# Kernel optimization log

Measured on AMD Instinct MI355X. Metric: run time of the kernel, lower is better.

Reference implementation:

```python
import jax, jax.numpy as jnp
import numpy as np

WIDTH = 11
SIGMA = 5.0
C1 = 0.01 ** 2
C2 = 0.02 ** 2
B, C, H, W = 16, 3, 512, 512


def _gaussian_kernel(n_channel):
    # Matches torch module: exp(-x^2/(2 sigma^2)) over arange(-width/2, width/2)
    g = np.exp(-1.0 * np.arange(-(WIDTH / 2), WIDTH / 2) ** 2 / (2 * SIGMA ** 2))
    g = np.outer(g, g.reshape(WIDTH, 1))
    g = g / np.sum(g)
    # Original kernel is block-diagonal [C, C, k, k] with w on the diagonal;
    # mathematically identical to a depthwise conv with kernel [C, 1, k, k].
    w = np.zeros((n_channel, 1, WIDTH, WIDTH), dtype=np.float32)
    w[:, 0] = g.astype(np.float32)
    return jnp.asarray(w)


def setup_inputs() -> dict:
    key = jax.random.key(0)
    k1, k2 = jax.random.split(key)
    inp = jax.random.normal(k1, (B, C, H, W), dtype=jnp.float32)
    tgt = jax.random.normal(k2, (B, C, H, W), dtype=jnp.float32)
    return {"input": inp, "target": tgt, "w": _gaussian_kernel(C)}


def reference(input, target, w):
    nb, nc = input.shape[0], input.shape[1]

    def blur(x):  # depthwise VALID conv == original block-diagonal dense conv
        return jax.lax.conv_general_dilated(
            x, w, window_strides=(1, 1), padding='VALID',
            dimension_numbers=('NCHW', 'OIHW', 'NCHW'),
            feature_group_count=nc)

    mux = blur(input)
    muy = blur(target)
    sigmax2 = blur(input * input) - mux * mux
    sigmay2 = blur(target * target) - muy * muy
    sigmaxy = blur(input * target) - mux * muy

    l = (2 * mux * muy + C1) / (mux * mux + muy * muy + C1)
    cs = (2 * sigmaxy + C2) / (sigmax2 + sigmay2 + C2)
    return 1 - jnp.sum(l * cs) / (nb * nc)
```

## Files before the change

kernel.cpp:

```cpp
#include <hip/hip_runtime.h>

typedef __attribute__((ext_vector_type(8))) _Float16 f16x8;
typedef __attribute__((ext_vector_type(4))) float f32x4;
typedef __attribute__((ext_vector_type(4))) _Float16 h4;
typedef __attribute__((ext_vector_type(2))) __fp16 hw2;
typedef __attribute__((ext_vector_type(2))) float v2f;

#define IMG 512
#define OUT_N 502
#define NPLANE 48
#define NBAND 32
#define NBLK (NBAND * NPLANE)
#define VP 520
#define C1c 0.0001f
#define C2c 0.0004f

union H8u { hw2 p[4]; f16x8 v; };
union H4u { hw2 p[2]; h4 v; };

__device__ __forceinline__ float ssim_px(float mx, float my, float P, float M) {
    float A = mx*mx, B = my*my, mxy = mx*my;
    float sumsq = 0.5f*(P+M) - A - B;
    float sxy   = 0.25f*(P-M) - mxy;
    float num = (2.f*mxy + C1c) * (2.f*sxy + C2c);
    float den = (A + B + C1c) * (sumsq + C2c);
    return num * __builtin_amdgcn_rcpf(den);
}

__device__ __forceinline__ float ssim_px2(v2f mx, v2f my, v2f P, v2f M) {
    v2f A = mx*mx, B = my*my, mxy = mx*my;
    v2f sumsq = 0.5f*(P+M) - A - B;
    v2f sxy   = 0.25f*(P-M) - mxy;
    v2f num = (2.f*mxy + C1c) * (2.f*sxy + C2c);
    v2f den = (A + B + C1c) * (sumsq + C2c);
    return num.x * __builtin_amdgcn_rcpf(den.x)
         + num.y * __builtin_amdgcn_rcpf(den.y);
}

__global__ __launch_bounds__(512, 2) void ssim_band(
    const float* __restrict__ in, const float* __restrict__ tgt,
    const float* __restrict__ w, float* __restrict__ partial)
{
    __shared__ __attribute__((aligned(16))) _Float16 vlds[4][16][VP];
    __shared__ float g1s[16];
    __shared__ float red[8];

    const int tid   = threadIdx.x;
    const int lane  = tid & 63;
    const int wv    = tid >> 6;
    const int f     = blockIdx.x;
    const int s     = ((f & 7) * (NBLK / 8)) + (f >> 3);
    const int band  = s & (NBAND - 1);
    const int plane = s >> 5;
    const int r0 = band * 16;
    const bool edge = (r0 + 16 > OUT_N);
    const float* __restrict__ ip = in  + (size_t)plane * (IMG*IMG);
    const float* __restrict__ tp = tgt + (size_t)plane * (IMG*IMG);

    const int fi = lane & 15;
    const int kg = lane >> 4;
    const int kB = kg * 8;

    int idx[8];
    #pragma unroll
    for (int q = 0; q < 8; ++q) {
        const int rr = min(r0 + kB + q, IMG - 1);
        idx[q] = rr * IMG + wv * 64 + fi;
    }

#define VLOAD(T, XS, YS) \
    { _Pragma("unroll") \
      for (int q = 0; q < 8; ++q) { \
          XS[q] = ip[idx[q] + 16*(T)]; \
          YS[q] = tp[idx[q] + 16*(T)]; \
      } }

    float xA[8], yA[8], xB[8], yB[8];
    VLOAD(0, xA, yA)
    VLOAD(1, xB, yB)

    if (tid < 11) {
        float ws_ = 0.f;
        #pragma unroll
        for (int j = 0; j < 11; ++j) ws_ += w[tid*11 + j];
        g1s[tid] = ws_;
    }
    __syncthreads();
    float g[11];
    #pragma unroll
    for (int j = 0; j < 11; ++j)
        g[j] = __int_as_float(__builtin_amdgcn_readfirstlane(__float_as_int(g1s[j])));

    f16x8 band_f;
    #pragma unroll
    for (int q = 0; q < 8; ++q) {
        float wq = 0.f;
        #pragma unroll
        for (int j = 0; j <= 10; ++j)
            wq = (kB + q - fi == j) ? g[j] : wq;
        band_f[q] = (_Float16)wq;
    }

    float acc = 0.f;
    const f32x4 z = {0.f, 0.f, 0.f, 0.f};

#define VSTORE(F, D) \
    { H4u u_; \
      u_.p[0] = __builtin_amdgcn_cvt_pkrtz((D)[0], (D)[1]); \
      u_.p[1] = __builtin_amdgcn_cvt_pkrtz((D)[2], (D)[3]); \
      *reinterpret_cast<h4*>(&vlds[F][fi][cb_]) = u_.v; }

#define VPROC(T, XS, YS) \
    { H8u ux, uy; \
      ux.p[0] = __builtin_amdgcn_cvt_pkrtz(XS[0], XS[1]); \
      ux.p[1] = __builtin_amdgcn_cvt_pkrtz(XS[2], XS[3]); \
      ux.p[2] = __builtin_amdgcn_cvt_pkrtz(XS[4], XS[5]); \
      ux.p[3] = __builtin_amdgcn_cvt_pkrtz(XS[6], XS[7]); \
      uy.p[0] = __builtin_amdgcn_cvt_pkrtz(YS[0], YS[1]); \
      uy.p[1] = __builtin_amdgcn_cvt_pkrtz(YS[2], YS[3]); \
      uy.p[2] = __builtin_amdgcn_cvt_pkrtz(YS[4], YS[5]); \
      uy.p[3] = __builtin_amdgcn_cvt_pkrtz(YS[6], YS[7]); \
      f16x8 fX = ux.v, fY = uy.v; \
      f16x8 fS = fX + fY, fD = fX - fY;       \
      f16x8 fP = fS * fS, fM = fD * fD;       \
      f32x4 dX = __builtin_amdgcn_mfma_f32_16x16x32_f16(fX, band_f, z, 0, 0, 0); \
      f32x4 dY = __builtin_amdgcn_mfma_f32_16x16x32_f16(fY, band_f, z, 0, 0, 0); \
      f32x4 dP = __builtin_amdgcn_mfma_f32_16x16x32_f16(fP, band_f, z, 0, 0, 0); \
      f32x4 dM = __builtin_amdgcn_mfma_f32_16x16x32_f16(fM, band_f, z, 0, 0, 0); \
      const int cb_ = (wv*4 + (T))*16 + kg*4; \
      VSTORE(0, dX) VSTORE(1, dY) VSTORE(2, dP) VSTORE(3, dM) }

    VPROC(0, xA, yA)
    VLOAD(2, xA, yA)
    VPROC(1, xB, yB)
    VLOAD(3, xB, yB)
    VPROC(2, xA, yA)
    VPROC(3, xB, yB)

    __syncthreads();

#define HPROC(T) \
    { const int c0_ = (wv*4 + (T))*16; \
      const int kb_ = min(c0_ + kB, IMG - 8); \
      f16x8 aX = *reinterpret_cast<const f16x8*>(&vlds[0][fi][kb_]); \
      f16x8 aY = *reinterpret_cast<const f16x8*>(&vlds[1][fi][kb_]); \
      f16x8 aP = *reinterpret_cast<const f16x8*>(&vlds[2][fi][kb_]); \
      f16x8 aM = *reinterpret_cast<const f16x8*>(&vlds[3][fi][kb_]); \
      f32x4 dX = __builtin_amdgcn_mfma_f32_16x16x32_f16(aX, band_f, z, 0, 0, 0); \
      f32x4 dY = __builtin_amdgcn_mfma_f32_16x16x32_f16(aY, band_f, z, 0, 0, 0); \
      f32x4 dP = __builtin_amdgcn_mfma_f32_16x16x32_f16(aP, band_f, z, 0, 0, 0); \
      f32x4 dM = __builtin_amdgcn_mfma_f32_16x16x32_f16(aM, band_f, z, 0, 0, 0); \
      const int oc = c0_ + fi; \
      if (oc < OUT_N) { \
          if (!edge) { \
              v2f mx0 = {dX[0], dX[1]}, my0 = {dY[0], dY[1]}; \
              v2f P0  = {dP[0], dP[1]}, M0  = {dM[0], dM[1]}; \
              v2f mx1 = {dX[2], dX[3]}, my1 = {dY[2], dY[3]}; \
              v2f P1  = {dP[2], dP[3]}, M1  = {dM[2], dM[3]}; \
              acc += ssim_px2(mx0, my0, P0, M0); \
              acc += ssim_px2(mx1, my1, P1, M1); \
          } else { \
              _Pragma("unroll") \
              for (int m = 0; m < 4; ++m) { \
                  const int oy = r0 + kg*4 + m; \
                  if (oy < OUT_N) \
                      acc += ssim_px(dX[m], dY[m], dP[m], dM[m]); \
              } \
          } } }

    HPROC(0) HPROC(1) HPROC(2) HPROC(3)

    #pragma unroll
    for (int off = 32; off > 0; off >>= 1)
        acc += __shfl_down(acc, off, 64);
    if (lane == 0) red[wv] = acc;
    __syncthreads();
    if (tid == 0) {
        float t = 0.f;
        #pragma unroll
        for (int i = 0; i < 8; ++i) t += red[i];
        partial[s] = t;
    }
}

__global__ __launch_bounds__(256) void ssim_final(
    const float* __restrict__ partial, int n, float* __restrict__ out)
{
    __shared__ double red[256];
    double s = 0.0;
    for (int i = threadIdx.x; i < n; i += 256) s += (double)partial[i];
    red[threadIdx.x] = s;
    __syncthreads();
    for (int off = 128; off > 0; off >>= 1) {
        if (threadIdx.x < off) red[threadIdx.x] += red[threadIdx.x + off];
        __syncthreads();
    }
    if (threadIdx.x == 0) out[0] = (float)(1.0 - red[0] / (double)NPLANE);
}

extern "C" void kernel_launch(void* const* d_in, const int* in_sizes, int n_in,
                              void* d_out, int out_size, void* d_ws, size_t ws_size,
                              hipStream_t stream) {
    const float* in  = (const float*)d_in[0];
    const float* tgt = (const float*)d_in[1];
    const float* wt  = (const float*)d_in[2];
    float* out  = (float*)d_out;
    float* part = (float*)d_ws;

    ssim_band<<<dim3(NBLK), 512, 0, stream>>>(in, tgt, wt, part);
    ssim_final<<<1, 256, 0, stream>>>(part, NBLK, out);
}
```

Baseline: 30.81 us.

## Tile into 64-column blocks with horizontal-first MFMA pass and vectorized loads

Splits each 16-row band into 8 column groups of 64, giving a grid eight times larger with 256-thread blocks. The horizontal blur now runs first on rows loaded with 16-byte vector loads, then the vertical blur reads back a small transposed LDS tile. This cuts LDS per block and is meant to raise occupancy and improve load coalescing. In exchange, each block now reloads the halo columns, and the final reduction has many more partial sums to add.

```diff
diff --git a/kernel.cpp b/kernel.cpp
--- a/kernel.cpp
+++ b/kernel.cpp
@@ -10,8 +10,9 @@
 #define OUT_N 502
 #define NPLANE 48
 #define NBAND 32
-#define NBLK (NBAND * NPLANE)
-#define VP 520
+#define NCG 8
+#define NBLK (NCG * NBAND * NPLANE)
+#define HP 40
 #define C1c 0.0001f
 #define C2c 0.0004f
 
@@ -37,22 +38,24 @@
          + num.y * __builtin_amdgcn_rcpf(den.y);
 }
 
-__global__ __launch_bounds__(512, 2) void ssim_band(
+__global__ __launch_bounds__(256, 3) void ssim_hf(
     const float* __restrict__ in, const float* __restrict__ tgt,
     const float* __restrict__ w, float* __restrict__ partial)
 {
-    __shared__ __attribute__((aligned(16))) _Float16 vlds[4][16][VP];
+    __shared__ __attribute__((aligned(16))) _Float16 hlds[4][64][HP];
     __shared__ float g1s[16];
-    __shared__ float red[8];
-
-    const int tid   = threadIdx.x;
-    const int lane  = tid & 63;
-    const int wv    = tid >> 6;
-    const int f     = blockIdx.x;
-    const int s     = ((f & 7) * (NBLK / 8)) + (f >> 3);
-    const int band  = s & (NBAND - 1);
-    const int plane = s >> 5;
+    __shared__ float red[4];
+
+    const int tid  = threadIdx.x;
+    const int lane = tid & 63;
+    const int wv   = tid >> 6;
+    const int f    = blockIdx.x;
+    const int s    = ((f & 7) * (NBLK / 8)) + (f >> 3);
+    const int cg   = s & 7;
+    const int band = (s >> 3) & (NBAND - 1);
+    const int plane = s >> 8;
     const int r0 = band * 16;
+    const int c0 = cg * 64;
     const bool edge = (r0 + 16 > OUT_N);
     const float* __restrict__ ip = in  + (size_t)plane * (IMG*IMG);
     const float* __restrict__ tp = tgt + (size_t)plane * (IMG*IMG);
@@ -61,23 +64,21 @@
     const int kg = lane >> 4;
     const int kB = kg * 8;
 
-    int idx[8];
-    #pragma unroll
-    for (int q = 0; q < 8; ++q) {
-        const int rr = min(r0 + kB + q, IMG - 1);
-        idx[q] = rr * IMG + wv * 64 + fi;
-    }
-
-#define VLOAD(T, XS, YS) \
-    { _Pragma("unroll") \
-      for (int q = 0; q < 8; ++q) { \
-          XS[q] = ip[idx[q] + 16*(T)]; \
-          YS[q] = tp[idx[q] + 16*(T)]; \
-      } }
-
-    float xA[8], yA[8], xB[8], yB[8];
-    VLOAD(0, xA, yA)
-    VLOAD(1, xB, yB)
+    const int p0 = 2*wv,     c_0 = p0 >> 2, t_0 = p0 & 3;
+    const int p1 = 2*wv + 1, c_1 = p1 >> 2, t_1 = p1 & 3;
+    const int row0 = min(r0 + 16*c_0 + fi, IMG - 1);
+    const int row1 = min(r0 + 16*c_1 + fi, IMG - 1);
+    const int cb0  = min(c0 + 16*t_0 + kB, IMG - 8);
+    const int cb1  = min(c0 + 16*t_1 + kB, IMG - 8);
+
+    const f32x4 xa0 = *(const f32x4*)(ip + row0*IMG + cb0);
+    const f32x4 xb0 = *(const f32x4*)(ip + row0*IMG + cb0 + 4);
+    const f32x4 ya0 = *(const f32x4*)(tp + row0*IMG + cb0);
+    const f32x4 yb0 = *(const f32x4*)(tp + row0*IMG + cb0 + 4);
+    const f32x4 xa1 = *(const f32x4*)(ip + row1*IMG + cb1);
+    const f32x4 xb1 = *(const f32x4*)(ip + row1*IMG + cb1 + 4);
+    const f32x4 ya1 = *(const f32x4*)(tp + row1*IMG + cb1);
+    const f32x4 yb1 = *(const f32x4*)(tp + row1*IMG + cb1 + 4);
 
     if (tid < 11) {
         float ws_ = 0.f;
@@ -101,86 +102,78 @@
         band_f[q] = (_Float16)wq;
     }
 
-    float acc = 0.f;
     const f32x4 z = {0.f, 0.f, 0.f, 0.f};
 
-#define VSTORE(F, D) \
+#define HSTORE(F, D) \
     { H4u u_; \
       u_.p[0] = __builtin_amdgcn_cvt_pkrtz((D)[0], (D)[1]); \
       u_.p[1] = __builtin_amdgcn_cvt_pkrtz((D)[2], (D)[3]); \
-      *reinterpret_cast<h4*>(&vlds[F][fi][cb_]) = u_.v; }
-
-#define VPROC(T, XS, YS) \
+      *reinterpret_cast<h4*>(&hlds[F][colL][rowL]) = u_.v; }
+
+#define HPROC(XA, XB, YA, YB, CC, TT) \
     { H8u ux, uy; \
-      ux.p[0] = __builtin_amdgcn_cvt_pkrtz(XS[0], XS[1]); \
-      ux.p[1] = __builtin_amdgcn_cvt_pkrtz(XS[2], XS[3]); \
-      ux.p[2] = __builtin_amdgcn_cvt_pkrtz(XS[4], XS[5]); \
-      ux.p[3] = __builtin_amdgcn_cvt_pkrtz(XS[6], XS[7]); \
-      uy.p[0] = __builtin_amdgcn_cvt_pkrtz(YS[0], YS[1]); \
-      uy.p[1] = __builtin_amdgcn_cvt_pkrtz(YS[2], YS[3]); \
-      uy.p[2] = __builtin_amdgcn_cvt_pkrtz(YS[4], YS[5]); \
-      uy.p[3] = __builtin_amdgcn_cvt_pkrtz(YS[6], YS[7]); \
+      ux.p[0] = __builtin_amdgcn_cvt_pkrtz((XA)[0], (XA)[1]); \
+      ux.p[1] = __builtin_amdgcn_cvt_pkrtz((XA)[2], (XA)[3]); \
+      ux.p[2] = __builtin_amdgcn_cvt_pkrtz((XB)[0], (XB)[1]); \
+      ux.p[3] = __builtin_amdgcn_cvt_pkrtz((XB)[2], (XB)[3]); \
+      uy.p[0] = __builtin_amdgcn_cvt_pkrtz((YA)[0], (YA)[1]); \
+      uy.p[1] = __builtin_amdgcn_cvt_pkrtz((YA)[2], (YA)[3]); \
+      uy.p[2] = __builtin_amdgcn_cvt_pkrtz((YB)[0], (YB)[1]); \
+      uy.p[3] = __builtin_amdgcn_cvt_pkrtz((YB)[2], (YB)[3]); \
       f16x8 fX = ux.v, fY = uy.v; \
-      f16x8 fS = fX + fY, fD = fX - fY;       \
-      f16x8 fP = fS * fS, fM = fD * fD;       \
+      f16x8 fS = fX + fY, fD = fX - fY; \
+      f16x8 fP = fS * fS, fM = fD * fD; \
       f32x4 dX = __builtin_amdgcn_mfma_f32_16x16x32_f16(fX, band_f, z, 0, 0, 0); \
       f32x4 dY = __builtin_amdgcn_mfma_f32_16x16x32_f16(fY, band_f, z, 0, 0, 0); \
       f32x4 dP = __builtin_amdgcn_mfma_f32_16x16x32_f16(fP, band_f, z, 0, 0, 0); \
       f32x4 dM = __builtin_amdgcn_mfma_f32_16x16x32_f16(fM, band_f, z, 0, 0, 0); \
-      const int cb_ = (wv*4 + (T))*16 + kg*4; \
-      VSTORE(0, dX) VSTORE(1, dY) VSTORE(2, dP) VSTORE(3, dM) }
-
-    VPROC(0, xA, yA)
-    VLOAD(2, xA, yA)
-    VPROC(1, xB, yB)
-    VLOAD(3, xB, yB)
-    VPROC(2, xA, yA)
-    VPROC(3, xB, yB)
-
-    __syncthreads();
-
-#define HPROC(T) \
-    { const int c0_ = (wv*4 + (T))*16; \
-      const int kb_ = min(c0_ + kB, IMG - 8); \
-      f16x8 aX = *reinterpret_cast<const f16x8*>(&vlds[0][fi][kb_]); \
-      f16x8 aY = *reinterpret_cast<const f16x8*>(&vlds[1][fi][kb_]); \
-      f16x8 aP = *reinterpret_cast<const f16x8*>(&vlds[2][fi][kb_]); \
-      f16x8 aM = *reinterpret_cast<const f16x8*>(&vlds[3][fi][kb_]); \
-      f32x4 dX = __builtin_amdgcn_mfma_f32_16x16x32_f16(aX, band_f, z, 0, 0, 0); \
-      f32x4 dY = __builtin_amdgcn_mfma_f32_16x16x32_f16(aY, band_f, z, 0, 0, 0); \
-      f32x4 dP = __builtin_amdgcn_mfma_f32_16x16x32_f16(aP, band_f, z, 0, 0, 0); \
-      f32x4 dM = __builtin_amdgcn_mfma_f32_16x16x32_f16(aM, band_f, z, 0, 0, 0); \
-      const int oc = c0_ + fi; \
-      if (oc < OUT_N) { \
-          if (!edge) { \
-              v2f mx0 = {dX[0], dX[1]}, my0 = {dY[0], dY[1]}; \
-              v2f P0  = {dP[0], dP[1]}, M0  = {dM[0], dM[1]}; \
-              v2f mx1 = {dX[2], dX[3]}, my1 = {dY[2], dY[3]}; \
-              v2f P1  = {dP[2], dP[3]}, M1  = {dM[2], dM[3]}; \
-              acc += ssim_px2(mx0, my0, P0, M0); \
-              acc += ssim_px2(mx1, my1, P1, M1); \
-          } else { \
-              _Pragma("unroll") \
-              for (int m = 0; m < 4; ++m) { \
-                  const int oy = r0 + kg*4 + m; \
-                  if (oy < OUT_N) \
-                      acc += ssim_px(dX[m], dY[m], dP[m], dM[m]); \
-              } \
-          } } }
-
-    HPROC(0) HPROC(1) HPROC(2) HPROC(3)
+      const int colL = 16*(TT) + fi;         \
+      const int rowL = 16*(CC) + 4*kg;       \
+      HSTORE(0, dX) HSTORE(1, dY) HSTORE(2, dP) HSTORE(3, dM) }
+
+    HPROC(xa0, xb0, ya0, yb0, c_0, t_0)
+    HPROC(xa1, xb1, ya1, yb1, c_1, t_1)
+
+    __syncthreads();
+
+    float acc = 0.f;
+    {
+        const int colL = 16*wv + fi;
+        f16x8 bX = *reinterpret_cast<const f16x8*>(&hlds[0][colL][kB]);
+        f16x8 bY = *reinterpret_cast<const f16x8*>(&hlds[1][colL][kB]);
+        f16x8 bP = *reinterpret_cast<const f16x8*>(&hlds[2][colL][kB]);
+        f16x8 bM = *reinterpret_cast<const f16x8*>(&hlds[3][colL][kB]);
+        f32x4 dX = __builtin_amdgcn_mfma_f32_16x16x32_f16(band_f, bX, z, 0, 0, 0);
+        f32x4 dY = __builtin_amdgcn_mfma_f32_16x16x32_f16(band_f, bY, z, 0, 0, 0);
+        f32x4 dP = __builtin_amdgcn_mfma_f32_16x16x32_f16(band_f, bP, z, 0, 0, 0);
+        f32x4 dM = __builtin_amdgcn_mfma_f32_16x16x32_f16(band_f, bM, z, 0, 0, 0);
+        const int oc = c0 + colL;
+        if (oc < OUT_N) {
+            if (!edge) {
+                v2f mx0 = {dX[0], dX[1]}, my0 = {dY[0], dY[1]};
+                v2f P0  = {dP[0], dP[1]}, M0  = {dM[0], dM[1]};
+                v2f mx1 = {dX[2], dX[3]}, my1 = {dY[2], dY[3]};
+                v2f P1  = {dP[2], dP[3]}, M1  = {dM[2], dM[3]};
+                acc += ssim_px2(mx0, my0, P0, M0);
+                acc += ssim_px2(mx1, my1, P1, M1);
+            } else {
+                #pragma unroll
+                for (int m = 0; m < 4; ++m) {
+                    const int oy = r0 + kg*4 + m;
+                    if (oy < OUT_N)
+                        acc += ssim_px(dX[m], dY[m], dP[m], dM[m]);
+                }
+            }
+        }
+    }
 
     #pragma unroll
     for (int off = 32; off > 0; off >>= 1)
         acc += __shfl_down(acc, off, 64);
     if (lane == 0) red[wv] = acc;
     __syncthreads();
-    if (tid == 0) {
-        float t = 0.f;
-        #pragma unroll
-        for (int i = 0; i < 8; ++i) t += red[i];
-        partial[s] = t;
-    }
+    if (tid == 0)
+        partial[s] = red[0] + red[1] + red[2] + red[3];
 }
 
 __global__ __launch_bounds__(256) void ssim_final(
@@ -207,6 +200,6 @@
     float* out  = (float*)d_out;
     float* part = (float*)d_ws;
 
-    ssim_band<<<dim3(NBLK), 512, 0, stream>>>(in, tgt, wt, part);
+    ssim_hf<<<dim3(NBLK), 256, 0, stream>>>(in, tgt, wt, part);
     ssim_final<<<1, 256, 0, stream>>>(part, NBLK, out);
 }
```

Result: slower. 64.67 us (+109.9%).
